# Optimization experiments

Measured on AMD Instinct MI355X. Metric: run time of the kernel, lower is better.

The kernel has to match this reference:

```python
import jax, jax.numpy as jnp
import numpy as np

B = 65536  # batch size

def setup_inputs() -> dict:
    key = jax.random.key(0)
    ks = jax.random.split(key, 6)
    x = jax.random.normal(ks[0], (B, 784), dtype=jnp.float32)
    conv_w = jax.random.normal(ks[1], (3, 3), dtype=jnp.float32) * 0.1
    in_size = (28 - 3 + 1) * (28 - 3 + 1)  # 676
    w1 = jax.random.normal(ks[2], (in_size, 300), dtype=jnp.float32) * 0.05
    b1 = jax.random.normal(ks[3], (300,), dtype=jnp.float32) * 0.05
    w2 = jax.random.normal(ks[4], (300, 10), dtype=jnp.float32) * 0.05
    b2 = jax.random.normal(ks[5], (10,), dtype=jnp.float32) * 0.05
    return {"x": x, "conv_w": conv_w, "w1": w1, "b1": b1, "w2": w2, "b2": b2}

def _convolve(img, conv_w):
    # img: [B,28,28]; conv_w: [kh,kw]. Valid cross-correlation (tensordot of each
    # window with the un-flipped kernel), matching the original Convolve().
    out = jax.lax.conv_general_dilated(
        img[:, None, :, :],            # [B,1,28,28]  NCHW
        conv_w[None, None, :, :],      # [1,1,3,3]    OIHW (no flip -> cross-correlation)
        window_strides=(1, 1),
        padding="VALID",
        dimension_numbers=("NCHW", "OIHW", "NCHW"),
    )
    return out[:, 0]  # [B,26,26]

def reference(x, conv_w, w1, b1, w2, b2):
    b = x.shape[0]
    img = x.reshape(b, 28, 28)
    feat = _convolve(img, conv_w).reshape(b, -1)      # [B,676]
    h1 = jax.nn.relu(feat @ w1 + b1)                  # [B,300]
    return h1 @ w2 + b2                               # [B,10]
```

## Files before the change

### kernel.cpp

```cpp
#include <hip/hip_runtime.h>
#include <hip/hip_bf16.h>

typedef __attribute__((ext_vector_type(8))) short bf16x8;
typedef __attribute__((ext_vector_type(4))) float f32x4;
typedef __attribute__((ext_vector_type(4))) unsigned int u32x4;
typedef unsigned short u16;
typedef unsigned int u32;

static constexpr int KDIM  = 784;
static constexpr int KP    = 800;
static constexpr int NDIM  = 300;
static constexpr int NP    = 320;
static constexpr int DDIM  = 10;
static constexpr int BM    = 256;
static constexpr int BK    = 64;
static constexpr int NFULL = 12;
static constexpr int H1STR = 328;
static constexpr int NROW  = 65536;
static constexpr int NTHR  = 512;
static constexpr int AU    = 16384;
static constexpr int BBASEU= 32768;
static constexpr int BU    = 20480;

__device__ __forceinline__ u16 f2bf(float f) {
  unsigned u = __builtin_bit_cast(unsigned, f);
  u += 0x7fffu + ((u >> 16) & 1u);
  return (u16)(u >> 16);
}
__device__ __forceinline__ u32 pk2(float a, float b) {
  u32 r;
  asm("v_cvt_pk_bf16_f32 %0, %1, %2" : "=v"(r) : "v"(a), "v"(b));
  return r;
}
__device__ __forceinline__ void gll16(const void* g, void* l) {
  __builtin_amdgcn_global_load_lds(
      (const __attribute__((address_space(1))) void*)g,
      (__attribute__((address_space(3))) void*)l, 16, 0, 0);
}

__global__ void build_weff(const float* __restrict__ cw,
                           const float* __restrict__ w1,
                           u16* __restrict__ weff) {
  int idx = blockIdx.x * 256 + threadIdx.x;
  if (idx >= NP * KP) return;
  int n = idx / KP;
  int k = idx - n * KP;
  float acc = 0.f;
  if (n < NDIM && k < KDIM) {
    int r = k / 28, c = k - (k / 28) * 28;
    #pragma unroll
    for (int dr = 0; dr < 3; ++dr) {
      int orr = r - dr;
      if ((unsigned)orr < 26u) {
        #pragma unroll
        for (int dc = 0; dc < 3; ++dc) {
          int oc = c - dc;
          if ((unsigned)oc < 26u)
            acc += cw[dr * 3 + dc] * w1[(orr * 26 + oc) * NDIM + n];
        }
      }
    }
  }
  weff[n * KP + k] = f2bf(acc);
}

__global__ void __launch_bounds__(NTHR, 2)
fused_mlp(const float* __restrict__ x, const float* __restrict__ b1,
          const float* __restrict__ w2, const float* __restrict__ b2,
          const u16* __restrict__ weff, float* __restrict__ out) {
  __shared__ __align__(16) u16 lds[73728];

  const int tid  = threadIdx.x;
  const int wv   = tid >> 6;
  const int lane = tid & 63;
  const int l16  = lane & 15;
  const int lhi  = lane >> 4;
  const int wm   = wv >> 2;
  const int wn   = wv & 3;
  const int bm   = blockIdx.x * BM;
  const int wvn  = wn * 80;

  int aR[4], aOg[4];
  #pragma unroll
  for (int j = 0; j < 4; ++j) {
    int p = tid + j * NTHR;
    aR[j]  = p >> 3;
    aOg[j] = (p & 7) ^ (aR[j] & 7);
  }
  int bN[5], bOg[5];
  #pragma unroll
  for (int i = 0; i < 5; ++i) {
    int s = tid + i * NTHR;
    bN[i]  = s >> 3;
    bOg[i] = (s & 7) ^ (bN[i] & 7);
  }

  f32x4 av[4][2];

  auto aload = [&](int t) {
    int k0 = t * BK;
    #pragma unroll
    for (int j = 0; j < 4; ++j) {
      int k = k0 + aOg[j] * 8;
      if (k + 8 > KDIM) k = k0;
      const float* g = x + (size_t)(bm + aR[j]) * KDIM + k;
      av[j][0] = *reinterpret_cast<const f32x4*>(g);
      av[j][1] = *reinterpret_cast<const f32x4*>(g + 4);
    }
  };
  auto cvtwrite = [&](int t) {
    u16* Ab = lds + (t & 1) * AU;
    #pragma unroll
    for (int j = 0; j < 4; ++j) {
      int p = tid + j * NTHR;
      u32x4 q = { pk2(av[j][0][0], av[j][0][1]), pk2(av[j][0][2], av[j][0][3]),
                  pk2(av[j][1][0], av[j][1][1]), pk2(av[j][1][2], av[j][1][3]) };
      *reinterpret_cast<u32x4*>(Ab + p * 8) = q;
    }
  };
  auto stageB = [&](int t) {
    char* base = (char*)(lds + BBASEU + (t & 1) * BU);
    int k0 = t * BK;
    #pragma unroll
    for (int i = 0; i < 5; ++i) {
      int k = k0 + bOg[i] * 8;
      if (k + 8 > KP) k = k0;
      gll16(weff + (size_t)bN[i] * KP + k, base + (tid + i * NTHR) * 16);
    }
  };

  f32x4 acc[8][5];
  #pragma unroll
  for (int mi = 0; mi < 8; ++mi)
    #pragma unroll
    for (int ni = 0; ni < 5; ++ni)
      acc[mi][ni] = (f32x4){0.f, 0.f, 0.f, 0.f};

  auto compute = [&](int t, int kk) {
    const u16* Ab = lds + (t & 1) * AU;
    const u16* Bb = lds + BBASEU + (t & 1) * BU;
    const int o = kk * 4 + lhi;
    bf16x8 bfr[5];
    #pragma unroll
    for (int ni = 0; ni < 5; ++ni) {
      int n = wvn + ni * 16 + l16;
      bfr[ni] = *reinterpret_cast<const bf16x8*>(Bb + (n * 8 + (o ^ (n & 7))) * 8);
    }
    #pragma unroll
    for (int mi = 0; mi < 8; ++mi) {
      int R = wm * 128 + mi * 16 + l16;
      bf16x8 am = *reinterpret_cast<const bf16x8*>(Ab + (R * 8 + (o ^ (R & 7))) * 8);
      #pragma unroll
      for (int ni = 0; ni < 5; ++ni)
        acc[mi][ni] = __builtin_amdgcn_mfma_f32_16x16x32_bf16(am, bfr[ni], acc[mi][ni], 0, 0, 0);
    }
  };

  aload(0);
  __builtin_amdgcn_sched_barrier(0);
  stageB(0);
  __builtin_amdgcn_sched_barrier(0);
  asm volatile("s_waitcnt vmcnt(5)" ::: "memory");
  cvtwrite(0);
  asm volatile("s_waitcnt vmcnt(0) lgkmcnt(0)" ::: "memory");
  __builtin_amdgcn_s_barrier();
  __builtin_amdgcn_sched_barrier(0);

  for (int t = 0; t < NFULL; ++t) {
    aload(t + 1);
    __builtin_amdgcn_sched_barrier(0);
    stageB(t + 1);
    __builtin_amdgcn_sched_barrier(0);
    compute(t, 0);
    __builtin_amdgcn_sched_barrier(0);
    asm volatile("s_waitcnt vmcnt(5)" ::: "memory");
    cvtwrite(t + 1);
    __builtin_amdgcn_sched_barrier(0);
    compute(t, 1);
    __builtin_amdgcn_sched_barrier(0);
    asm volatile("s_waitcnt vmcnt(0) lgkmcnt(0)" ::: "memory");
    __builtin_amdgcn_s_barrier();
    __builtin_amdgcn_sched_barrier(0);
  }
  compute(NFULL, 0);
  __syncthreads();

  u16* H1  = lds;
  u16* W2T = lds + 20992;

  for (int i = tid; i < 16 * NP; i += NTHR) {
    int d = i / NP, n = i - (i / NP) * NP;
    float v = (d < DDIM && n < NDIM) ? w2[n * DDIM + d] : 0.f;
    W2T[d * H1STR + n] = f2bf(v);
  }
  float biasv[5];
  #pragma unroll
  for (int ni = 0; ni < 5; ++ni) {
    int col = wvn + ni * 16 + l16;
    biasv[ni] = (col < NDIM) ? b1[col] : 0.f;
  }

  #pragma unroll
  for (int p = 0; p < 4; ++p) {
    if (wm == (p >> 1)) {
      #pragma unroll
      for (int mj = 0; mj < 4; ++mj) {
        int mi = (p & 1) * 4 + mj;
        #pragma unroll
        for (int ni = 0; ni < 5; ++ni) {
          int col = wvn + ni * 16 + l16;
          int rb  = mj * 16 + lhi * 4;
          #pragma unroll
          for (int r = 0; r < 4; ++r) {
            float h = acc[mi][ni][r] + biasv[ni];
            H1[(rb + r) * H1STR + col] = f2bf(fmaxf(h, 0.f));
          }
        }
      }
    }
    __syncthreads();
    if (wv < 4) {
      f32x4 a2c = (f32x4){0.f, 0.f, 0.f, 0.f};
      #pragma unroll
      for (int ks = 0; ks < NP / 32; ++ks) {
        bf16x8 a2 = *reinterpret_cast<const bf16x8*>(
            H1 + (wv * 16 + l16) * H1STR + ks * 32 + lhi * 8);
        bf16x8 bw = *reinterpret_cast<const bf16x8*>(
            W2T + l16 * H1STR + ks * 32 + lhi * 8);
        a2c = __builtin_amdgcn_mfma_f32_16x16x32_bf16(a2, bw, a2c, 0, 0, 0);
      }
      if (l16 < DDIM) {
        float bb = b2[l16];
        #pragma unroll
        for (int r = 0; r < 4; ++r) {
          int row = bm + p * 64 + wv * 16 + lhi * 4 + r;
          out[(size_t)row * DDIM + l16] = a2c[r] + bb;
        }
      }
    }
    __syncthreads();
  }
}

extern "C" void kernel_launch(void* const* d_in, const int* in_sizes, int n_in,
                              void* d_out, int out_size, void* d_ws, size_t ws_size,
                              hipStream_t stream) {
  const float* x  = (const float*)d_in[0];
  const float* cw = (const float*)d_in[1];
  const float* w1 = (const float*)d_in[2];
  const float* b1 = (const float*)d_in[3];
  const float* w2 = (const float*)d_in[4];
  const float* b2 = (const float*)d_in[5];
  float* out = (float*)d_out;
  u16* weff = (u16*)d_ws;

  hipLaunchKernelGGL(build_weff, dim3((NP * KP + 255) / 256), dim3(256), 0, stream,
                     cw, w1, weff);
  hipLaunchKernelGGL(fused_mlp, dim3(NROW / BM), dim3(NTHR), 0, stream,
                     x, b1, w2, b2, weff, out);
}
```

Before: 69.62 us.

## Shrink tile to 128 rows, BK=32, triple-buffer A with padded LDS rows

Halves the block to 128 rows and 256 threads with a 32-wide K step, so each block uses far less LDS and more blocks can be resident per CU. A moves to a three-stage ring buffer, loaded two steps ahead, with padded row stride instead of XOR swizzle. The kernel now runs 25 K steps with one compute per step, in place of 12 steps plus a tail. This trades more loop iterations and barriers per block for higher occupancy and deeper prefetch, and risks more LDS bank conflicts from the padded stride.

```diff
diff --git a/kernel.cpp b/kernel.cpp
--- a/kernel.cpp
+++ b/kernel.cpp
@@ -12,15 +12,16 @@
 static constexpr int NDIM  = 300;
 static constexpr int NP    = 320;
 static constexpr int DDIM  = 10;
-static constexpr int BM    = 256;
-static constexpr int BK    = 64;
-static constexpr int NFULL = 12;
+static constexpr int BM    = 128;
+static constexpr int BK    = 32;
+static constexpr int NSTEP = 25;
 static constexpr int H1STR = 328;
 static constexpr int NROW  = 65536;
-static constexpr int NTHR  = 512;
-static constexpr int AU    = 16384;
-static constexpr int BBASEU= 32768;
-static constexpr int BU    = 20480;
+static constexpr int NTHR  = 256;
+static constexpr int ASTR  = 36;
+static constexpr int AU    = 128 * ASTR;
+static constexpr int BBASEU= 3 * AU;
+static constexpr int BU    = 10240;
 
 __device__ __forceinline__ u16 f2bf(float f) {
   unsigned u = __builtin_bit_cast(unsigned, f);
@@ -68,65 +69,54 @@
 fused_mlp(const float* __restrict__ x, const float* __restrict__ b1,
           const float* __restrict__ w2, const float* __restrict__ b2,
           const u16* __restrict__ weff, float* __restrict__ out) {
-  __shared__ __align__(16) u16 lds[73728];
+  __shared__ __align__(16) u16 lds[34304];
 
   const int tid  = threadIdx.x;
   const int wv   = tid >> 6;
   const int lane = tid & 63;
   const int l16  = lane & 15;
   const int lhi  = lane >> 4;
-  const int wm   = wv >> 2;
-  const int wn   = wv & 3;
   const int bm   = blockIdx.x * BM;
-  const int wvn  = wn * 80;
-
-  int aR[4], aOg[4];
-  #pragma unroll
-  for (int j = 0; j < 4; ++j) {
-    int p = tid + j * NTHR;
-    aR[j]  = p >> 3;
-    aOg[j] = (p & 7) ^ (aR[j] & 7);
-  }
-  int bN[5], bOg[5];
+  const int wvn  = wv * 80;
+
+  const int rA = tid >> 1, hA = tid & 1;
+  const float* xrowA = x + (size_t)(bm + rA) * KDIM;
+
+  int bRow[5], bQg[5];
   #pragma unroll
   for (int i = 0; i < 5; ++i) {
     int s = tid + i * NTHR;
-    bN[i]  = s >> 3;
-    bOg[i] = (s & 7) ^ (bN[i] & 7);
-  }
-
-  f32x4 av[4][2];
-
+    bRow[i] = s >> 2;
+    bQg[i]  = (s & 3) ^ (bRow[i] & 3);
+  }
+
+  f32x4 av[4];
   auto aload = [&](int t) {
-    int k0 = t * BK;
-    #pragma unroll
-    for (int j = 0; j < 4; ++j) {
-      int k = k0 + aOg[j] * 8;
-      if (k + 8 > KDIM) k = k0;
-      const float* g = x + (size_t)(bm + aR[j]) * KDIM + k;
-      av[j][0] = *reinterpret_cast<const f32x4*>(g);
-      av[j][1] = *reinterpret_cast<const f32x4*>(g + 4);
-    }
+    int k0 = (t < NSTEP) ? t * BK : 0;
+    int kk = k0 + hA * 16;
+    if (kk > KDIM - 16) kk = KDIM - 16;
+    const float* g = xrowA + kk;
+    av[0] = *reinterpret_cast<const f32x4*>(g);
+    av[1] = *reinterpret_cast<const f32x4*>(g + 4);
+    av[2] = *reinterpret_cast<const f32x4*>(g + 8);
+    av[3] = *reinterpret_cast<const f32x4*>(g + 12);
   };
   auto cvtwrite = [&](int t) {
-    u16* Ab = lds + (t & 1) * AU;
-    #pragma unroll
-    for (int j = 0; j < 4; ++j) {
-      int p = tid + j * NTHR;
-      u32x4 q = { pk2(av[j][0][0], av[j][0][1]), pk2(av[j][0][2], av[j][0][3]),
-                  pk2(av[j][1][0], av[j][1][1]), pk2(av[j][1][2], av[j][1][3]) };
-      *reinterpret_cast<u32x4*>(Ab + p * 8) = q;
-    }
+    u16* Ab = lds + (t % 3) * AU + rA * ASTR + hA * 16;
+    u32x4 q0 = { pk2(av[0][0], av[0][1]), pk2(av[0][2], av[0][3]),
+                 pk2(av[1][0], av[1][1]), pk2(av[1][2], av[1][3]) };
+    u32x4 q1 = { pk2(av[2][0], av[2][1]), pk2(av[2][2], av[2][3]),
+                 pk2(av[3][0], av[3][1]), pk2(av[3][2], av[3][3]) };
+    *reinterpret_cast<u32x4*>(Ab)     = q0;
+    *reinterpret_cast<u32x4*>(Ab + 8) = q1;
   };
   auto stageB = [&](int t) {
     char* base = (char*)(lds + BBASEU + (t & 1) * BU);
-    int k0 = t * BK;
-    #pragma unroll
-    for (int i = 0; i < 5; ++i) {
-      int k = k0 + bOg[i] * 8;
-      if (k + 8 > KP) k = k0;
-      gll16(weff + (size_t)bN[i] * KP + k, base + (tid + i * NTHR) * 16);
-    }
+    int k0 = (t < NSTEP) ? t * BK : 0;
+    #pragma unroll
+    for (int i = 0; i < 5; ++i)
+      gll16(weff + (size_t)bRow[i] * KP + k0 + bQg[i] * 8,
+            base + (tid + i * NTHR) * 16);
   };
 
   f32x4 acc[8][5];
@@ -136,20 +126,20 @@
     for (int ni = 0; ni < 5; ++ni)
       acc[mi][ni] = (f32x4){0.f, 0.f, 0.f, 0.f};
 
-  auto compute = [&](int t, int kk) {
-    const u16* Ab = lds + (t & 1) * AU;
+  auto compute = [&](int t) {
+    const u16* Ab = lds + (t % 3) * AU;
     const u16* Bb = lds + BBASEU + (t & 1) * BU;
-    const int o = kk * 4 + lhi;
     bf16x8 bfr[5];
     #pragma unroll
     for (int ni = 0; ni < 5; ++ni) {
       int n = wvn + ni * 16 + l16;
-      bfr[ni] = *reinterpret_cast<const bf16x8*>(Bb + (n * 8 + (o ^ (n & 7))) * 8);
+      int slot = n * 4 + (lhi ^ (n & 3));
+      bfr[ni] = *reinterpret_cast<const bf16x8*>(Bb + slot * 8);
     }
     #pragma unroll
     for (int mi = 0; mi < 8; ++mi) {
-      int R = wm * 128 + mi * 16 + l16;
-      bf16x8 am = *reinterpret_cast<const bf16x8*>(Ab + (R * 8 + (o ^ (R & 7))) * 8);
+      int R = mi * 16 + l16;
+      bf16x8 am = *reinterpret_cast<const bf16x8*>(Ab + R * ASTR + lhi * 8);
       #pragma unroll
       for (int ni = 0; ni < 5; ++ni)
         acc[mi][ni] = __builtin_amdgcn_mfma_f32_16x16x32_bf16(am, bfr[ni], acc[mi][ni], 0, 0, 0);
@@ -158,31 +148,32 @@
 
   aload(0);
   __builtin_amdgcn_sched_barrier(0);
+  asm volatile("s_waitcnt vmcnt(0)" ::: "memory");
+  cvtwrite(0);
+  aload(1);
+  __builtin_amdgcn_sched_barrier(0);
   stageB(0);
   __builtin_amdgcn_sched_barrier(0);
   asm volatile("s_waitcnt vmcnt(5)" ::: "memory");
-  cvtwrite(0);
+  cvtwrite(1);
   asm volatile("s_waitcnt vmcnt(0) lgkmcnt(0)" ::: "memory");
   __builtin_amdgcn_s_barrier();
   __builtin_amdgcn_sched_barrier(0);
 
-  for (int t = 0; t < NFULL; ++t) {
-    aload(t + 1);
+  for (int t = 0; t < NSTEP; ++t) {
+    aload(t + 2);
     __builtin_amdgcn_sched_barrier(0);
     stageB(t + 1);
     __builtin_amdgcn_sched_barrier(0);
-    compute(t, 0);
+    compute(t);
     __builtin_amdgcn_sched_barrier(0);
     asm volatile("s_waitcnt vmcnt(5)" ::: "memory");
-    cvtwrite(t + 1);
-    __builtin_amdgcn_sched_barrier(0);
-    compute(t, 1);
+    cvtwrite(t + 2);
     __builtin_amdgcn_sched_barrier(0);
     asm volatile("s_waitcnt vmcnt(0) lgkmcnt(0)" ::: "memory");
     __builtin_amdgcn_s_barrier();
     __builtin_amdgcn_sched_barrier(0);
   }
-  compute(NFULL, 0);
   __syncthreads();
 
   u16* H1  = lds;
@@ -201,25 +192,23 @@
   }
 
   #pragma unroll
-  for (int p = 0; p < 4; ++p) {
-    if (wm == (p >> 1)) {
+  for (int p = 0; p < 2; ++p) {
+    #pragma unroll
+    for (int mj = 0; mj < 4; ++mj) {
+      int mi = p * 4 + mj;
       #pragma unroll
-      for (int mj = 0; mj < 4; ++mj) {
-        int mi = (p & 1) * 4 + mj;
+      for (int ni = 0; ni < 5; ++ni) {
+        int col = wvn + ni * 16 + l16;
+        int rb  = mj * 16 + lhi * 4;
         #pragma unroll
-        for (int ni = 0; ni < 5; ++ni) {
-          int col = wvn + ni * 16 + l16;
-          int rb  = mj * 16 + lhi * 4;
-          #pragma unroll
-          for (int r = 0; r < 4; ++r) {
-            float h = acc[mi][ni][r] + biasv[ni];
-            H1[(rb + r) * H1STR + col] = f2bf(fmaxf(h, 0.f));
-          }
+        for (int r = 0; r < 4; ++r) {
+          float h = acc[mi][ni][r] + biasv[ni];
+          H1[(rb + r) * H1STR + col] = f2bf(fmaxf(h, 0.f));
         }
       }
     }
     __syncthreads();
-    if (wv < 4) {
+    {
       f32x4 a2c = (f32x4){0.f, 0.f, 0.f, 0.f};
       #pragma unroll
       for (int ks = 0; ks < NP / 32; ++ks) {
```

Measured after the change: 89.16 us. +28.1%, slower.
